# Performance work log

Measured on AMD Instinct MI355X. Metric: run time of the kernel, lower is better.

Reference implementation:

```python
import jax, jax.numpy as jnp
import numpy as np

EPS = 1e-12  # torch F.normalize eps

def rmsnorm(x, g, dim):
    # F.normalize(x, dim=-1) * sqrt(dim) * g  (g is a learned scalar)
    n = jnp.maximum(jnp.linalg.norm(x, axis=-1, keepdims=True), EPS)
    return x / n * (dim ** 0.5) * g

def modulate(x, scale, shift):
    # x: (B,T,D); scale/shift: (B,D)
    return x * (1.0 + scale[:, None, :]) + shift[:, None, :]

def setup_inputs() -> dict:
    key = jax.random.key(0)
    ks = jax.random.split(key, 12)
    B, T, D, H = 8, 1024, 1024, 16
    Dm = 4 * D
    s = 0.02
    inp = {
        'x': jax.random.normal(ks[0], (B, T, D), jnp.float32),
        'c': jax.random.normal(ks[1], (B, D), jnp.float32),
        'g1': jnp.ones((1,), jnp.float32),
        'g2': jnp.ones((1,), jnp.float32),
        'gq': jnp.ones((1,), jnp.float32),
        'gk': jnp.ones((1,), jnp.float32),
        'Wqkv': jax.random.normal(ks[2], (3 * D, D), jnp.float32) * s,
        'bqkv': jnp.zeros((3 * D,), jnp.float32),
        'Wproj': jax.random.normal(ks[3], (D, D), jnp.float32) * s,
        'bproj': jnp.zeros((D,), jnp.float32),
        'Wfc1': jax.random.normal(ks[4], (Dm, D), jnp.float32) * s,
        'bfc1': jnp.zeros((Dm,), jnp.float32),
        'Wfc2': jax.random.normal(ks[5], (D, Dm), jnp.float32) * s,
        'bfc2': jnp.zeros((D,), jnp.float32),
        'Wada': jax.random.normal(ks[6], (6 * D, D), jnp.float32) * s,
        'bada': jnp.zeros((6 * D,), jnp.float32),
    }
    return inp

def reference(x, c, g1, g2, gq, gk, Wqkv, bqkv, Wproj, bproj,
              Wfc1, bfc1, Wfc2, bfc2, Wada, bada):
    B, T, D = x.shape
    H = 16
    hd = D // H

    # adaLN modulation: SiLU -> Linear -> chunk 6 along last dim
    ada = jax.nn.silu(c) @ Wada.T + bada  # (B, 6D)
    shift_msa, scale_msa, gate_msa, shift_mlp, scale_mlp, gate_mlp = jnp.split(ada, 6, axis=-1)

    # --- attention branch ---
    h = modulate(rmsnorm(x, g1, D), scale_msa, shift_msa)  # (B,T,D)
    qkv = h @ Wqkv.T + bqkv  # (B,T,3D)
    qkv = qkv.reshape(B, T, 3, H, hd).transpose(2, 0, 3, 1, 4)  # (3,B,H,T,hd)
    q, k, v = qkv[0], qkv[1], qkv[2]
    q = rmsnorm(q, gq, hd) * (hd ** -0.5)
    k = rmsnorm(k, gk, hd)
    attn = jax.nn.softmax(jnp.einsum('bhqd,bhkd->bhqk', q, k), axis=-1)
    o = jnp.einsum('bhqk,bhkd->bhqd', attn, v)  # (B,H,T,hd)
    o = o.transpose(0, 2, 1, 3).reshape(B, T, D)
    o = o @ Wproj.T + bproj
    x = x + gate_msa[:, None, :] * o

    # --- MLP branch ---
    h = modulate(rmsnorm(x, g2, D), scale_mlp, shift_mlp)
    h = jax.nn.gelu(h @ Wfc1.T + bfc1, approximate=True)
    h = h @ Wfc2.T + bfc2
    x = x + gate_mlp[:, None, :] * h
    return x
```

## Files before the change

### kernel.cpp

```cpp
#include <hip/hip_runtime.h>
#include <hip/hip_bf16.h>
#include <math.h>

typedef __bf16 bf16x8 __attribute__((ext_vector_type(8)));
typedef __bf16 bf16x4 __attribute__((ext_vector_type(4)));
typedef float  f32x4  __attribute__((ext_vector_type(4)));

#define DEV static __device__ __forceinline__

DEV unsigned short f2bf(float f) {
    unsigned u = __builtin_bit_cast(unsigned, f);
    u += 0x7fffu + ((u >> 16) & 1u);
    return (unsigned short)(u >> 16);
}
DEV float bf2f(unsigned short u) {
    unsigned x = ((unsigned)u) << 16;
    return __builtin_bit_cast(float, x);
}

__global__ void k_cvtall(const float* __restrict__ a, const float* __restrict__ b,
                         const float* __restrict__ c, const float* __restrict__ d,
                         unsigned short* __restrict__ oa, unsigned short* __restrict__ ob,
                         unsigned short* __restrict__ oc, unsigned short* __restrict__ od) {
    size_t i = (size_t)blockIdx.x * 1024 + threadIdx.x * 4;
    const float* src; unsigned short* dst; size_t off;
    if (i < 3145728)      { src = a; dst = oa; off = i; }
    else if (i < 4194304) { src = b; dst = ob; off = i - 3145728; }
    else if (i < 8388608) { src = c; dst = oc; off = i - 4194304; }
    else                  { src = d; dst = od; off = i - 8388608; }
    float4 v = *(const float4*)(src + off);
    ushort4 o;
    o.x = f2bf(v.x); o.y = f2bf(v.y); o.z = f2bf(v.z); o.w = f2bf(v.w);
    *(ushort4*)(dst + off) = o;
}

__global__ void k_ada(const float* __restrict__ c, const float* __restrict__ Wada,
                      const float* __restrict__ bada, float* __restrict__ ada) {
    __shared__ float sc[1024];
    int b = blockIdx.x;
    int tid = threadIdx.x;
    for (int k = tid; k < 1024; k += 256) {
        float x = c[b * 1024 + k];
        sc[k] = x / (1.f + __expf(-x));
    }
    __syncthreads();
    int wid = tid >> 6, lane = tid & 63;
    int n = blockIdx.y * 4 + wid;
    const float* wr = Wada + (size_t)n * 1024;
    float acc = 0.f;
    #pragma unroll
    for (int k = 0; k < 1024; k += 64) acc += sc[k + lane] * wr[k + lane];
    #pragma unroll
    for (int o = 32; o; o >>= 1) acc += __shfl_xor(acc, o);
    if (lane == 0) ada[b * 6144 + n] = acc + bada[n];
}

__global__ void k_norm_mod(const float* __restrict__ x, const float* __restrict__ ada,
                           const float* __restrict__ g, unsigned short* __restrict__ h,
                           int shift_off, int scale_off) {
    int row = blockIdx.x;
    int b = row >> 10;
    int tid = threadIdx.x;
    float4 v = *(const float4*)(x + (size_t)row * 1024 + tid * 4);
    float ss = v.x * v.x + v.y * v.y + v.z * v.z + v.w * v.w;
    #pragma unroll
    for (int o = 32; o; o >>= 1) ss += __shfl_xor(ss, o);
    __shared__ float red[4];
    int wid = tid >> 6, lane = tid & 63;
    if (lane == 0) red[wid] = ss;
    __syncthreads();
    float nrm = sqrtf(red[0] + red[1] + red[2] + red[3]);
    float f = g[0] * 32.f / fmaxf(nrm, 1e-12f);
    float4 s4 = *(const float4*)(ada + b * 6144 + scale_off + tid * 4);
    float4 h4 = *(const float4*)(ada + b * 6144 + shift_off + tid * 4);
    ushort4 o;
    o.x = f2bf(v.x * f * (1.f + s4.x) + h4.x);
    o.y = f2bf(v.y * f * (1.f + s4.y) + h4.y);
    o.z = f2bf(v.z * f * (1.f + s4.z) + h4.z);
    o.w = f2bf(v.w * f * (1.f + s4.w) + h4.w);
    *(ushort4*)(h + (size_t)row * 1024 + tid * 4) = o;
}

template <int EPI>
__global__ __launch_bounds__(256, 4)
void k_gemm5(const unsigned short* __restrict__ A, const unsigned short* __restrict__ Bw,
             const float* __restrict__ bias, int N, int K, int gridM, int gridN, int Kc,
             unsigned short* __restrict__ outH,
             const float* __restrict__ gq, const float* __restrict__ gk) {
    __shared__ unsigned short lA[128 * 64];
    __shared__ unsigned short lB[128 * 64];
    int tid = threadIdx.x;
    int wid = tid >> 6, lane = tid & 63;
    int li = lane & 15, lg = lane >> 4;
    int bid = blockIdx.x;
    int mb = bid % gridM;
    int nb = (bid / gridM) % gridN;
    int sp = bid / (gridM * gridN);
    int m0 = mb * 128, n0 = nb * 128;
    int k0 = sp * Kc;
    int wr = (wid >> 1) * 64, wc = (wid & 1) * 64;

    int trow = tid >> 3;
    int gcol = ((tid & 7) ^ (trow & 7)) * 8;
    int sl0 = (lg ^ (li & 7)) * 8;
    int sl1 = ((4 + lg) ^ (li & 7)) * 8;

    f32x4 acc[4][4] = {};

    for (int kk = 0; kk < Kc; kk += 64) {
        #pragma unroll
        for (int l = 0; l < 4; ++l) {
            int row = l * 32 + trow;
            const unsigned short* ga = A  + (size_t)(m0 + row) * K + k0 + kk + gcol;
            const unsigned short* gb = Bw + (size_t)(n0 + row) * K + k0 + kk + gcol;
            unsigned short* la = lA + (l * 256 + wid * 64) * 8;
            unsigned short* lb = lB + (l * 256 + wid * 64) * 8;
            __builtin_amdgcn_global_load_lds((const __attribute__((address_space(1))) void*)ga,
                                             (__attribute__((address_space(3))) void*)la, 16, 0, 0);
            __builtin_amdgcn_global_load_lds((const __attribute__((address_space(1))) void*)gb,
                                             (__attribute__((address_space(3))) void*)lb, 16, 0, 0);
        }
        __syncthreads();
        bf16x8 af[4], bfr[4];
        #pragma unroll
        for (int i = 0; i < 4; ++i)
            af[i] = *(const bf16x8*)(lA + (wr + i * 16 + li) * 64 + sl0);
        #pragma unroll
        for (int j = 0; j < 4; ++j)
            bfr[j] = *(const bf16x8*)(lB + (wc + j * 16 + li) * 64 + sl0);
        #pragma unroll
        for (int i = 0; i < 4; ++i)
            #pragma unroll
            for (int j = 0; j < 4; ++j)
                acc[i][j] = __builtin_amdgcn_mfma_f32_16x16x32_bf16(af[i], bfr[j], acc[i][j], 0, 0, 0);
        #pragma unroll
        for (int i = 0; i < 4; ++i)
            af[i] = *(const bf16x8*)(lA + (wr + i * 16 + li) * 64 + sl1);
        #pragma unroll
        for (int j = 0; j < 4; ++j)
            bfr[j] = *(const bf16x8*)(lB + (wc + j * 16 + li) * 64 + sl1);
        #pragma unroll
        for (int i = 0; i < 4; ++i)
            #pragma unroll
            for (int j = 0; j < 4; ++j)
                acc[i][j] = __builtin_amdgcn_mfma_f32_16x16x32_bf16(af[i], bfr[j], acc[i][j], 0, 0, 0);
        __syncthreads();
    }

    int rb4 = lg * 4;
    size_t poff = (size_t)sp * ((size_t)8192 * N);
    if (EPI == 5) {
        int typ = n0 >> 10;
        if (typ == 2) {
            #pragma unroll
            for (int i = 0; i < 4; ++i)
                #pragma unroll
                for (int j = 0; j < 4; ++j)
                    #pragma unroll
                    for (int r = 0; r < 4; ++r) {
                        int row = m0 + wr + i * 16 + rb4 + r;
                        int col = n0 + wc + j * 16 + li;
                        outH[(size_t)row * N + col] = f2bf(acc[i][j][r] + bias[col]);
                    }
        } else {
            float gsc = (typ == 0) ? gq[0] : 8.f * gk[0];
            #pragma unroll
            for (int i = 0; i < 4; ++i) {
                #pragma unroll
                for (int j = 0; j < 4; ++j)
                    #pragma unroll
                    for (int r = 0; r < 4; ++r)
                        acc[i][j][r] += bias[n0 + wc + j * 16 + li];
                float scl[4];
                #pragma unroll
                for (int r = 0; r < 4; ++r) {
                    float s = acc[i][0][r] * acc[i][0][r] + acc[i][1][r] * acc[i][1][r]
                            + acc[i][2][r] * acc[i][2][r] + acc[i][3][r] * acc[i][3][r];
                    s += __shfl_xor(s, 1);
                    s += __shfl_xor(s, 2);
                    s += __shfl_xor(s, 4);
                    s += __shfl_xor(s, 8);
                    scl[r] = gsc / fmaxf(sqrtf(s), 1e-12f);
                }
                #pragma unroll
                for (int j = 0; j < 4; ++j)
                    #pragma unroll
                    for (int r = 0; r < 4; ++r) {
                        int row = m0 + wr + i * 16 + rb4 + r;
                        int col = n0 + wc + j * 16 + li;
                        outH[(size_t)row * N + col] = f2bf(acc[i][j][r] * scl[r]);
                    }
            }
        }
        return;
    }
    #pragma unroll
    for (int i = 0; i < 4; ++i) {
        #pragma unroll
        for (int j = 0; j < 4; ++j) {
            #pragma unroll
            for (int r = 0; r < 4; ++r) {
                int row = m0 + wr + i * 16 + rb4 + r;
                int col = n0 + wc + j * 16 + li;
                if (EPI == 0) {
                    outH[(size_t)row * N + col] = f2bf(acc[i][j][r] + bias[col]);
                } else if (EPI == 2) {
                    float vv = acc[i][j][r] + bias[col];
                    float a2 = 0.7978845608f * (vv + 0.044715f * vv * vv * vv);
                    float e = __expf(-2.f * fabsf(a2));
                    float th = copysignf((1.f - e) / (1.f + e), a2);
                    outH[(size_t)row * N + col] = f2bf(0.5f * vv * (1.f + th));
                } else {
                    outH[poff + (size_t)row * N + col] = f2bf(acc[i][j][r]);
                }
            }
        }
    }
}

__global__ void k_fix_norm(const float* __restrict__ x, const unsigned short* __restrict__ P,
                           const float* __restrict__ bias, const float* __restrict__ ada,
                           const float* __restrict__ g2, float* __restrict__ out,
                           unsigned short* __restrict__ h2) {
    int row = blockIdx.x, b = row >> 10, tid = threadIdx.x;
    int c = tid * 4;
    size_t base = (size_t)row * 1024 + c;
    ushort4 p0 = *(const ushort4*)(P + base);
    ushort4 p1 = *(const ushort4*)(P + 8388608 + base);
    float4 xv = *(const float4*)(x + base);
    float4 bi = *(const float4*)(bias + c);
    float4 gt = *(const float4*)(ada + b * 6144 + 2048 + c);
    float4 v;
    v.x = xv.x + gt.x * (bf2f(p0.x) + bf2f(p1.x) + bi.x);
    v.y = xv.y + gt.y * (bf2f(p0.y) + bf2f(p1.y) + bi.y);
    v.z = xv.z + gt.z * (bf2f(p0.z) + bf2f(p1.z) + bi.z);
    v.w = xv.w + gt.w * (bf2f(p0.w) + bf2f(p1.w) + bi.w);
    *(float4*)(out + base) = v;
    float ss = v.x * v.x + v.y * v.y + v.z * v.z + v.w * v.w;
    #pragma unroll
    for (int o = 32; o; o >>= 1) ss += __shfl_xor(ss, o);
    __shared__ float red[4];
    int wid = tid >> 6, lane = tid & 63;
    if (lane == 0) red[wid] = ss;
    __syncthreads();
    float nrm = sqrtf(red[0] + red[1] + red[2] + red[3]);
    float f = g2[0] * 32.f / fmaxf(nrm, 1e-12f);
    float4 sc = *(const float4*)(ada + b * 6144 + 4096 + c);
    float4 sh = *(const float4*)(ada + b * 6144 + 3072 + c);
    ushort4 o;
    o.x = f2bf(v.x * f * (1.f + sc.x) + sh.x);
    o.y = f2bf(v.y * f * (1.f + sc.y) + sh.y);
    o.z = f2bf(v.z * f * (1.f + sc.z) + sh.z);
    o.w = f2bf(v.w * f * (1.f + sc.w) + sh.w);
    *(ushort4*)(h2 + base) = o;
}

__global__ void k_fixf(const unsigned short* __restrict__ P, const float* __restrict__ bias,
                       const float* __restrict__ ada, float* __restrict__ out) {
    int row = blockIdx.x, b = row >> 10, tid = threadIdx.x;
    int c = tid * 4;
    size_t base = (size_t)row * 1024 + c;
    ushort4 p0 = *(const ushort4*)(P + base);
    ushort4 p1 = *(const ushort4*)(P + 8388608 + base);
    float4 xv = *(const float4*)(out + base);
    float4 bi = *(const float4*)(bias + c);
    float4 gt = *(const float4*)(ada + b * 6144 + 5120 + c);
    float4 v;
    v.x = xv.x + gt.x * (bf2f(p0.x) + bf2f(p1.x) + bi.x);
    v.y = xv.y + gt.y * (bf2f(p0.y) + bf2f(p1.y) + bi.y);
    v.z = xv.z + gt.z * (bf2f(p0.z) + bf2f(p1.z) + bi.z);
    v.w = xv.w + gt.w * (bf2f(p0.w) + bf2f(p1.w) + bi.w);
    *(float4*)(out + base) = v;
}

__global__ __launch_bounds__(256)
void k_vt(const unsigned short* __restrict__ qkv, unsigned short* __restrict__ Vtg) {
    __shared__ unsigned short vt[64 * 72];
    int bh = blockIdx.x;
    int b = bh >> 4, h = bh & 15;
    int t0 = blockIdx.y * 64;
    int tid = threadIdx.x;
    int row = tid >> 2, part = tid & 3;
    size_t rbase = ((size_t)(b * 1024 + t0 + row)) * 3072 + 2048 + h * 64 + part * 16;
    uint4 u0 = *(const uint4*)(qkv + rbase);
    uint4 u1 = *(const uint4*)(qkv + rbase + 8);
    const unsigned* pu = (const unsigned*)&u0;
    #pragma unroll
    for (int j = 0; j < 4; ++j) {
        vt[(part * 16 + 2*j)     * 72 + row] = (unsigned short)(pu[j] & 0xffff);
        vt[(part * 16 + 2*j + 1) * 72 + row] = (unsigned short)(pu[j] >> 16);
    }
    pu = (const unsigned*)&u1;
    #pragma unroll
    for (int j = 0; j < 4; ++j) {
        vt[(part * 16 + 8 + 2*j)     * 72 + row] = (unsigned short)(pu[j] & 0xffff);
        vt[(part * 16 + 8 + 2*j + 1) * 72 + row] = (unsigned short)(pu[j] >> 16);
    }
    __syncthreads();
    int d = tid >> 2, seg = tid & 3;
    uint4 w0 = *(const uint4*)(vt + d * 72 + seg * 16);
    uint4 w1 = *(const uint4*)(vt + d * 72 + seg * 16 + 8);
    size_t vdst = (size_t)bh * 65536 + (size_t)d * 1024 + t0 + seg * 16;
    *(uint4*)(Vtg + vdst)     = w0;
    *(uint4*)(Vtg + vdst + 8) = w1;
}

__global__ __launch_bounds__(256)
void k_attn3(const unsigned short* __restrict__ qkv,
             const unsigned short* __restrict__ Vtg,
             unsigned short* __restrict__ outp) {
    __shared__ unsigned short Kt[128 * 64];
    __shared__ unsigned short Vl[64 * 136];
    int bh = blockIdx.x;
    int b = bh >> 4, h = bh & 15;
    int t0 = blockIdx.y * 64;
    int tid = threadIdx.x, wid = tid >> 6, lane = tid & 63;
    int li = lane & 15, lg = lane >> 4;
    const size_t bh64k = (size_t)bh * 65536;

    bf16x8 q0, q1;
    {
        int qrow = b * 1024 + t0 + wid * 16 + li;
        const unsigned short* Qg = qkv + (size_t)qrow * 3072 + h * 64 + lg * 8;
        q0 = *(const bf16x8*)Qg;
        q1 = *(const bf16x8*)(Qg + 32);
    }
    f32x4 oacc[4] = {};
    float den = 0.f;

    for (int kt = 0; kt < 8; ++kt) {
        __syncthreads();
        #pragma unroll
        for (int i = 0; i < 4; ++i) {
            int s = i * 256 + tid;
            int r = s >> 3, c16 = s & 7;
            const unsigned short* src = qkv + (size_t)(b * 1024 + kt * 128 + r) * 3072
                                        + 1024 + h * 64 + ((c16 ^ (r & 7)) * 8);
            unsigned short* dst = Kt + i * 2048 + wid * 512;
            __builtin_amdgcn_global_load_lds((const __attribute__((address_space(1))) void*)src,
                                             (__attribute__((address_space(3))) void*)dst, 16, 0, 0);
        }
        #pragma unroll
        for (int i = 0; i < 4; ++i) {
            int s = i * 256 + tid;
            int d = s >> 4, k16 = s & 15;
            uint4 v = *(const uint4*)(Vtg + bh64k + (size_t)d * 1024 + kt * 128 + k16 * 8);
            *(uint4*)(Vl + d * 136 + k16 * 8) = v;
        }
        __syncthreads();

        f32x4 st[8];
        #pragma unroll
        for (int f = 0; f < 8; ++f) {
            int row = f * 16 + li;
            bf16x8 a0 = *(const bf16x8*)(Kt + row * 64 + ((lg       ^ (row & 7)) * 8));
            bf16x8 a1 = *(const bf16x8*)(Kt + row * 64 + (((4 + lg) ^ (row & 7)) * 8));
            f32x4 s = {};
            s = __builtin_amdgcn_mfma_f32_16x16x32_bf16(a0, q0, s, 0, 0, 0);
            s = __builtin_amdgcn_mfma_f32_16x16x32_bf16(a1, q1, s, 0, 0, 0);
            f32x4 e;
            e[0] = __expf(s[0]); e[1] = __expf(s[1]);
            e[2] = __expf(s[2]); e[3] = __expf(s[3]);
            den += e[0] + e[1] + e[2] + e[3];
            st[f] = e;
        }
        #pragma unroll
        for (int ks = 0; ks < 4; ++ks) {
            f32x4 e0 = st[2 * ks], e1 = st[2 * ks + 1];
            bf16x8 pa;
            pa[0] = (__bf16)e0[0]; pa[1] = (__bf16)e0[1]; pa[2] = (__bf16)e0[2]; pa[3] = (__bf16)e0[3];
            pa[4] = (__bf16)e1[0]; pa[5] = (__bf16)e1[1]; pa[6] = (__bf16)e1[2]; pa[7] = (__bf16)e1[3];
            #pragma unroll
            for (int df = 0; df < 4; ++df) {
                const unsigned short* vp = Vl + (df * 16 + li) * 136 + ks * 32 + lg * 4;
                bf16x4 v0 = *(const bf16x4*)vp;
                bf16x4 v1 = *(const bf16x4*)(vp + 16);
                bf16x8 vb = __builtin_shufflevector(v0, v1, 0, 1, 2, 3, 4, 5, 6, 7);
                oacc[df] = __builtin_amdgcn_mfma_f32_16x16x32_bf16(pa, vb, oacc[df], 0, 0, 0);
            }
        }
    }
    den += __shfl_xor(den, 16);
    den += __shfl_xor(den, 32);

    #pragma unroll
    for (int r2 = 0; r2 < 4; ++r2) {
        float dm = __shfl(den, lg * 4 + r2);
        float inv = 1.f / dm;
        int t = t0 + wid * 16 + lg * 4 + r2;
        #pragma unroll
        for (int df = 0; df < 4; ++df) {
            int col = h * 64 + df * 16 + li;
            outp[((size_t)(b * 1024 + t)) * 1024 + col] = f2bf(oacc[df][r2] * inv);
        }
    }
}

extern "C" void kernel_launch(void* const* d_in, const int* in_sizes, int n_in,
                              void* d_out, int out_size, void* d_ws, size_t ws_size,
                              hipStream_t stream) {
    const float* x     = (const float*)d_in[0];
    const float* c     = (const float*)d_in[1];
    const float* g1    = (const float*)d_in[2];
    const float* g2    = (const float*)d_in[3];
    const float* gq    = (const float*)d_in[4];
    const float* gk    = (const float*)d_in[5];
    const float* Wqkv  = (const float*)d_in[6];
    const float* bqkv  = (const float*)d_in[7];
    const float* Wproj = (const float*)d_in[8];
    const float* bproj = (const float*)d_in[9];
    const float* Wfc1  = (const float*)d_in[10];
    const float* bfc1  = (const float*)d_in[11];
    const float* Wfc2  = (const float*)d_in[12];
    const float* bfc2  = (const float*)d_in[13];
    const float* Wada  = (const float*)d_in[14];
    const float* bada  = (const float*)d_in[15];
    float* out = (float*)d_out;

    char* ws = (char*)d_ws;
    unsigned short* wqkv_bf = (unsigned short*)ws; ws += (size_t)3072 * 1024 * 2;
    unsigned short* wproj_bf= (unsigned short*)ws; ws += (size_t)1024 * 1024 * 2;
    unsigned short* wfc1_bf = (unsigned short*)ws; ws += (size_t)4096 * 1024 * 2;
    unsigned short* wfc2_bf = (unsigned short*)ws; ws += (size_t)4096 * 1024 * 2;
    float* ada = (float*)ws;                       ws += (size_t)8 * 6144 * 4;
    unsigned short* hbuf = (unsigned short*)ws;    ws += (size_t)8192 * 1024 * 2;
    unsigned short* qkvb16 = (unsigned short*)ws;  ws += (size_t)8192 * 3072 * 2;
    unsigned short* Vtg = (unsigned short*)ws;     ws += (size_t)8192 * 64 * 16 * 2;
    unsigned short* Pbuf = (unsigned short*)ws;    ws += (size_t)2 * 8192 * 1024 * 2;
    unsigned short* fc1out = qkvb16;

    k_cvtall<<<12288, 256, 0, stream>>>(Wqkv, Wproj, Wfc1, Wfc2,
                                        wqkv_bf, wproj_bf, wfc1_bf, wfc2_bf);
    k_ada<<<dim3(8, 1536), 256, 0, stream>>>(c, Wada, bada, ada);
    k_norm_mod<<<8192, 256, 0, stream>>>(x, ada, g1, hbuf, 0, 1024);
    k_gemm5<5><<<1536, 256, 0, stream>>>(hbuf, wqkv_bf, bqkv, 3072, 1024, 64, 24, 1024,
                                         qkvb16, gq, gk);
    k_vt<<<dim3(128, 16), 256, 0, stream>>>(qkvb16, Vtg);
    k_attn3<<<dim3(128, 16), 256, 0, stream>>>(qkvb16, Vtg, hbuf);
    k_gemm5<4><<<1024, 256, 0, stream>>>(hbuf, wproj_bf, bproj, 1024, 1024, 64, 8, 512,
                                         Pbuf, nullptr, nullptr);
    k_fix_norm<<<8192, 256, 0, stream>>>(x, Pbuf, bproj, ada, g2, out, hbuf);
    k_gemm5<2><<<2048, 256, 0, stream>>>(hbuf, wfc1_bf, bfc1, 4096, 1024, 64, 32, 1024,
                                         fc1out, nullptr, nullptr);
    k_gemm5<4><<<1024, 256, 0, stream>>>(fc1out, wfc2_bf, bfc2, 1024, 4096, 64, 8, 2048,
                                         Pbuf, nullptr, nullptr);
    k_fixf<<<8192, 256, 0, stream>>>(Pbuf, bfc2, ada, out);
}
```

Before: 389.5 us.

## Add 256x256-tile GEMM with async global-to-LDS double buffering for QKV and MLP

Introduces a new GEMM kernel with 512 threads and 256x256 output tiles. It stages A and B directly from global memory into LDS using global_load_lds, double-buffered across K sub-tiles, and interleaves MFMA bursts at raised wave priority with the async staging. The kernel replaces the 128x128 GEMM for the QKV, FC1 and FC2 projections; the proj GEMM keeps the old kernel. The larger tiles are meant to improve operand reuse and hide global load latency. The trade-offs are fewer blocks (256–512) on a large-CU GPU, which risks lower occupancy and a tail wave, plus higher register pressure from 32 accumulators per thread.

```diff
diff --git a/kernel.cpp b/kernel.cpp
--- a/kernel.cpp
+++ b/kernel.cpp
@@ -82,11 +82,205 @@
 }
 
 template <int EPI>
+__global__ __launch_bounds__(512, 2)
+void k_gemm8(const unsigned short* __restrict__ A, const unsigned short* __restrict__ Bw,
+             const float* __restrict__ bias, int N, int K, int gridM, int gridN, int Kc,
+             unsigned short* __restrict__ outH,
+             const float* __restrict__ gq, const float* __restrict__ gk) {
+    __shared__ unsigned short sA[2][2][256 * 32];
+    __shared__ unsigned short sB[2][2][256 * 32];
+    int tid = threadIdx.x;
+    int wid = tid >> 6, lane = tid & 63;
+    int li = lane & 15, lg = lane >> 4;
+    int wm = wid >> 2, wn = wid & 3;
+    int bid = blockIdx.x;
+    int mb = bid % gridM;
+    int nb = (bid / gridM) % gridN;
+    int sp = bid / (gridM * gridN);
+    int m0 = mb * 256, n0 = nb * 256;
+    int k0 = sp * Kc;
+
+    int srow = tid >> 2, sslot = tid & 3;
+    int gs = (sslot ^ ((srow + (srow >> 2)) & 3)) * 8;
+    const unsigned short* Abase = A + (size_t)m0 * K + (size_t)srow * K + gs + k0;
+    const unsigned short* Bbase = Bw + (size_t)n0 * K + (size_t)srow * K + gs + k0;
+    size_t s128K = (size_t)128 * K;
+
+    int aoff[8], boff[4];
+    #pragma unroll
+    for (int mh = 0; mh < 2; ++mh)
+        #pragma unroll
+        for (int mf = 0; mf < 4; ++mf) {
+            int row = wm * 128 + mh * 64 + mf * 16 + li;
+            aoff[mh * 4 + mf] = row * 32 + ((lg ^ ((row + (row >> 2)) & 3)) * 8);
+        }
+    #pragma unroll
+    for (int nf = 0; nf < 4; ++nf) {
+        int row = wn * 64 + nf * 16 + li;
+        boff[nf] = row * 32 + ((lg ^ ((row + (row >> 2)) & 3)) * 8);
+    }
+
+    auto stageA = [&](int tile, int ks) {
+        unsigned short* reg = &sA[tile & 1][ks][0];
+        const unsigned short* src = Abase + tile * 64 + ks * 32;
+        __builtin_amdgcn_global_load_lds((const __attribute__((address_space(1))) void*)src,
+            (__attribute__((address_space(3))) void*)(reg + wid * 512), 16, 0, 0);
+        __builtin_amdgcn_global_load_lds((const __attribute__((address_space(1))) void*)(src + s128K),
+            (__attribute__((address_space(3))) void*)(reg + 4096 + wid * 512), 16, 0, 0);
+    };
+    auto stageB = [&](int tile, int ks) {
+        unsigned short* reg = &sB[tile & 1][ks][0];
+        const unsigned short* src = Bbase + tile * 64 + ks * 32;
+        __builtin_amdgcn_global_load_lds((const __attribute__((address_space(1))) void*)src,
+            (__attribute__((address_space(3))) void*)(reg + wid * 512), 16, 0, 0);
+        __builtin_amdgcn_global_load_lds((const __attribute__((address_space(1))) void*)(src + s128K),
+            (__attribute__((address_space(3))) void*)(reg + 4096 + wid * 512), 16, 0, 0);
+    };
+
+    int NT = Kc >> 6;
+    stageA(0, 0); stageB(0, 0); stageA(0, 1); stageB(0, 1); stageA(1, 0); stageB(1, 0);
+    asm volatile("s_waitcnt vmcnt(4)" ::: "memory");
+    __builtin_amdgcn_s_barrier();
+
+    f32x4 acc[8][4] = {};
+    bf16x8 bfr[4], afr[4];
+
+    for (int t = 0; t < NT; ++t) {
+        int buf = t & 1;
+        #pragma unroll
+        for (int nf = 0; nf < 4; ++nf) bfr[nf] = *(const bf16x8*)(&sB[buf][0][0] + boff[nf]);
+        #pragma unroll
+        for (int mf = 0; mf < 4; ++mf) afr[mf] = *(const bf16x8*)(&sA[buf][0][0] + aoff[mf]);
+        if (t + 1 < NT) stageA(t + 1, 1);
+        __builtin_amdgcn_s_barrier();
+        __builtin_amdgcn_s_setprio(1);
+        #pragma unroll
+        for (int mf = 0; mf < 4; ++mf)
+            #pragma unroll
+            for (int nf = 0; nf < 4; ++nf)
+                acc[mf][nf] = __builtin_amdgcn_mfma_f32_16x16x32_bf16(afr[mf], bfr[nf], acc[mf][nf], 0, 0, 0);
+        __builtin_amdgcn_s_setprio(0);
+        __builtin_amdgcn_s_barrier();
+        #pragma unroll
+        for (int mf = 0; mf < 4; ++mf) afr[mf] = *(const bf16x8*)(&sA[buf][0][0] + aoff[4 + mf]);
+        if (t + 1 < NT) stageB(t + 1, 1);
+        __builtin_amdgcn_s_barrier();
+        __builtin_amdgcn_s_setprio(1);
+        #pragma unroll
+        for (int mf = 0; mf < 4; ++mf)
+            #pragma unroll
+            for (int nf = 0; nf < 4; ++nf)
+                acc[4 + mf][nf] = __builtin_amdgcn_mfma_f32_16x16x32_bf16(afr[mf], bfr[nf], acc[4 + mf][nf], 0, 0, 0);
+        __builtin_amdgcn_s_setprio(0);
+        __builtin_amdgcn_s_barrier();
+        #pragma unroll
+        for (int nf = 0; nf < 4; ++nf) bfr[nf] = *(const bf16x8*)(&sB[buf][1][0] + boff[nf]);
+        #pragma unroll
+        for (int mf = 0; mf < 4; ++mf) afr[mf] = *(const bf16x8*)(&sA[buf][1][0] + aoff[mf]);
+        if (t + 2 < NT) stageA(t + 2, 0);
+        __builtin_amdgcn_s_barrier();
+        __builtin_amdgcn_s_setprio(1);
+        #pragma unroll
+        for (int mf = 0; mf < 4; ++mf)
+            #pragma unroll
+            for (int nf = 0; nf < 4; ++nf)
+                acc[mf][nf] = __builtin_amdgcn_mfma_f32_16x16x32_bf16(afr[mf], bfr[nf], acc[mf][nf], 0, 0, 0);
+        __builtin_amdgcn_s_setprio(0);
+        __builtin_amdgcn_s_barrier();
+        #pragma unroll
+        for (int mf = 0; mf < 4; ++mf) afr[mf] = *(const bf16x8*)(&sA[buf][1][0] + aoff[4 + mf]);
+        if (t + 2 < NT) stageB(t + 2, 0);
+        __builtin_amdgcn_s_barrier();
+        __builtin_amdgcn_s_setprio(1);
+        #pragma unroll
+        for (int mf = 0; mf < 4; ++mf)
+            #pragma unroll
+            for (int nf = 0; nf < 4; ++nf)
+                acc[4 + mf][nf] = __builtin_amdgcn_mfma_f32_16x16x32_bf16(afr[mf], bfr[nf], acc[4 + mf][nf], 0, 0, 0);
+        __builtin_amdgcn_s_setprio(0);
+        if (t < NT - 1) {
+            if (t + 2 < NT) asm volatile("s_waitcnt vmcnt(4)" ::: "memory");
+            else            asm volatile("s_waitcnt vmcnt(0)" ::: "memory");
+        }
+        __builtin_amdgcn_s_barrier();
+    }
+
+    int rb4 = lg * 4;
+    int wrb = m0 + wm * 128;
+    int wcb = n0 + wn * 64;
+    size_t poff = (size_t)sp * ((size_t)8192 * N);
+    if (EPI == 5) {
+        int typ = n0 >> 10;
+        if (typ == 2) {
+            #pragma unroll
+            for (int mf = 0; mf < 8; ++mf)
+                #pragma unroll
+                for (int nf = 0; nf < 4; ++nf)
+                    #pragma unroll
+                    for (int r = 0; r < 4; ++r) {
+                        int row = wrb + mf * 16 + rb4 + r;
+                        int col = wcb + nf * 16 + li;
+                        outH[(size_t)row * N + col] = f2bf(acc[mf][nf][r] + bias[col]);
+                    }
+        } else {
+            float gsc = (typ == 0) ? gq[0] : 8.f * gk[0];
+            #pragma unroll
+            for (int mf = 0; mf < 8; ++mf) {
+                #pragma unroll
+                for (int nf = 0; nf < 4; ++nf)
+                    #pragma unroll
+                    for (int r = 0; r < 4; ++r)
+                        acc[mf][nf][r] += bias[wcb + nf * 16 + li];
+                float scl[4];
+                #pragma unroll
+                for (int r = 0; r < 4; ++r) {
+                    float s = acc[mf][0][r] * acc[mf][0][r] + acc[mf][1][r] * acc[mf][1][r]
+                            + acc[mf][2][r] * acc[mf][2][r] + acc[mf][3][r] * acc[mf][3][r];
+                    s += __shfl_xor(s, 1);
+                    s += __shfl_xor(s, 2);
+                    s += __shfl_xor(s, 4);
+                    s += __shfl_xor(s, 8);
+                    scl[r] = gsc / fmaxf(sqrtf(s), 1e-12f);
+                }
+                #pragma unroll
+                for (int nf = 0; nf < 4; ++nf)
+                    #pragma unroll
+                    for (int r = 0; r < 4; ++r) {
+                        int row = wrb + mf * 16 + rb4 + r;
+                        int col = wcb + nf * 16 + li;
+                        outH[(size_t)row * N + col] = f2bf(acc[mf][nf][r] * scl[r]);
+                    }
+            }
+        }
+        return;
+    }
+    #pragma unroll
+    for (int mf = 0; mf < 8; ++mf) {
+        #pragma unroll
+        for (int nf = 0; nf < 4; ++nf) {
+            #pragma unroll
+            for (int r = 0; r < 4; ++r) {
+                int row = wrb + mf * 16 + rb4 + r;
+                int col = wcb + nf * 16 + li;
+                if (EPI == 2) {
+                    float vv = acc[mf][nf][r] + bias[col];
+                    float a2 = 0.7978845608f * (vv + 0.044715f * vv * vv * vv);
+                    float e = __expf(-2.f * fabsf(a2));
+                    float th = copysignf((1.f - e) / (1.f + e), a2);
+                    outH[(size_t)row * N + col] = f2bf(0.5f * vv * (1.f + th));
+                } else {
+                    outH[poff + (size_t)row * N + col] = f2bf(acc[mf][nf][r]);
+                }
+            }
+        }
+    }
+}
+
+template <int EPI>
 __global__ __launch_bounds__(256, 4)
 void k_gemm5(const unsigned short* __restrict__ A, const unsigned short* __restrict__ Bw,
              const float* __restrict__ bias, int N, int K, int gridM, int gridN, int Kc,
-             unsigned short* __restrict__ outH,
-             const float* __restrict__ gq, const float* __restrict__ gk) {
+             unsigned short* __restrict__ outH) {
     __shared__ unsigned short lA[128 * 64];
     __shared__ unsigned short lB[128 * 64];
     int tid = threadIdx.x;
@@ -149,51 +343,6 @@
 
     int rb4 = lg * 4;
     size_t poff = (size_t)sp * ((size_t)8192 * N);
-    if (EPI == 5) {
-        int typ = n0 >> 10;
-        if (typ == 2) {
-            #pragma unroll
-            for (int i = 0; i < 4; ++i)
-                #pragma unroll
-                for (int j = 0; j < 4; ++j)
-                    #pragma unroll
-                    for (int r = 0; r < 4; ++r) {
-                        int row = m0 + wr + i * 16 + rb4 + r;
-                        int col = n0 + wc + j * 16 + li;
-                        outH[(size_t)row * N + col] = f2bf(acc[i][j][r] + bias[col]);
-                    }
-        } else {
-            float gsc = (typ == 0) ? gq[0] : 8.f * gk[0];
-            #pragma unroll
-            for (int i = 0; i < 4; ++i) {
-                #pragma unroll
-                for (int j = 0; j < 4; ++j)
-                    #pragma unroll
-                    for (int r = 0; r < 4; ++r)
-                        acc[i][j][r] += bias[n0 + wc + j * 16 + li];
-                float scl[4];
-                #pragma unroll
-                for (int r = 0; r < 4; ++r) {
-                    float s = acc[i][0][r] * acc[i][0][r] + acc[i][1][r] * acc[i][1][r]
-                            + acc[i][2][r] * acc[i][2][r] + acc[i][3][r] * acc[i][3][r];
-                    s += __shfl_xor(s, 1);
-                    s += __shfl_xor(s, 2);
-                    s += __shfl_xor(s, 4);
-                    s += __shfl_xor(s, 8);
-                    scl[r] = gsc / fmaxf(sqrtf(s), 1e-12f);
-                }
-                #pragma unroll
-                for (int j = 0; j < 4; ++j)
-                    #pragma unroll
-                    for (int r = 0; r < 4; ++r) {
-                        int row = m0 + wr + i * 16 + rb4 + r;
-                        int col = n0 + wc + j * 16 + li;
-                        outH[(size_t)row * N + col] = f2bf(acc[i][j][r] * scl[r]);
-                    }
-            }
-        }
-        return;
-    }
     #pragma unroll
     for (int i = 0; i < 4; ++i) {
         #pragma unroll
@@ -204,12 +353,6 @@
                 int col = n0 + wc + j * 16 + li;
                 if (EPI == 0) {
                     outH[(size_t)row * N + col] = f2bf(acc[i][j][r] + bias[col]);
-                } else if (EPI == 2) {
-                    float vv = acc[i][j][r] + bias[col];
-                    float a2 = 0.7978845608f * (vv + 0.044715f * vv * vv * vv);
-                    float e = __expf(-2.f * fabsf(a2));
-                    float th = copysignf((1.f - e) / (1.f + e), a2);
-                    outH[(size_t)row * N + col] = f2bf(0.5f * vv * (1.f + th));
                 } else {
                     outH[poff + (size_t)row * N + col] = f2bf(acc[i][j][r]);
                 }
@@ -433,16 +576,15 @@
                                         wqkv_bf, wproj_bf, wfc1_bf, wfc2_bf);
     k_ada<<<dim3(8, 1536), 256, 0, stream>>>(c, Wada, bada, ada);
     k_norm_mod<<<8192, 256, 0, stream>>>(x, ada, g1, hbuf, 0, 1024);
-    k_gemm5<5><<<1536, 256, 0, stream>>>(hbuf, wqkv_bf, bqkv, 3072, 1024, 64, 24, 1024,
-                                         qkvb16, gq, gk);
+    k_gemm8<5><<<384, 512, 0, stream>>>(hbuf, wqkv_bf, bqkv, 3072, 1024, 32, 12, 1024,
+                                        qkvb16, gq, gk);
     k_vt<<<dim3(128, 16), 256, 0, stream>>>(qkvb16, Vtg);
     k_attn3<<<dim3(128, 16), 256, 0, stream>>>(qkvb16, Vtg, hbuf);
-    k_gemm5<4><<<1024, 256, 0, stream>>>(hbuf, wproj_bf, bproj, 1024, 1024, 64, 8, 512,
-                                         Pbuf, nullptr, nullptr);
+    k_gemm5<4><<<1024, 256, 0, stream>>>(hbuf, wproj_bf, bproj, 1024, 1024, 64, 8, 512, Pbuf);
     k_fix_norm<<<8192, 256, 0, stream>>>(x, Pbuf, bproj, ada, g2, out, hbuf);
-    k_gemm5<2><<<2048, 256, 0, stream>>>(hbuf, wfc1_bf, bfc1, 4096, 1024, 64, 32, 1024,
-                                         fc1out, nullptr, nullptr);
-    k_gemm5<4><<<1024, 256, 0, stream>>>(fc1out, wfc2_bf, bfc2, 1024, 4096, 64, 8, 2048,
-                                         Pbuf, nullptr, nullptr);
+    k_gemm8<2><<<512, 512, 0, stream>>>(hbuf, wfc1_bf, bfc1, 4096, 1024, 32, 16, 1024,
+                                        fc1out, nullptr, nullptr);
+    k_gemm8<4><<<256, 512, 0, stream>>>(fc1out, wfc2_bf, bfc2, 1024, 4096, 32, 4, 2048,
+                                        Pbuf, nullptr, nullptr);
     k_fixf<<<8192, 256, 0, stream>>>(Pbuf, bfc2, ada, out);
 }
```

New measurement: 430.0 us. 1.1x slower.
